# Performance work log

Measured on AMD Instinct MI355X. Metric: run time of the kernel, lower is better.

The kernel has to match this reference:

```python
import jax, jax.numpy as jnp
import numpy as np

B = 64        # number of graphs
NPG = 2048    # nodes per graph (equal-size; math identical to padded ragged original)
N = B * NPG
C = 64        # in_channels == out_channels
H = 4         # num_heads
D = 64        # out_channels per head


def setup_inputs() -> dict:
    key = jax.random.key(0)
    k1, k2, k3, k4, k5 = jax.random.split(key, 5)
    s = 1.0 / np.sqrt(C)
    return {
        "x": jax.random.normal(k1, (N, C), dtype=jnp.float32),
        "Wq_w": jax.random.uniform(k2, (H * D, C), jnp.float32, -s, s),
        "Wq_b": jax.random.uniform(k3, (H * D,), jnp.float32, -s, s),
        "Wk_w": jax.random.uniform(k4, (H * D, C), jnp.float32, -s, s),
        "Wk_b": jax.random.uniform(k5, (H * D,), jnp.float32, -s, s),
        "n_nodes": jnp.full((B,), NPG, dtype=jnp.int32),
    }


def reference(x, Wq_w, Wq_b, Wk_w, Wk_b, n_nodes):
    # Linear projections (torch Linear: x @ W^T + b), reshape to [N, H, D]
    q = (x @ Wq_w.T + Wq_b).reshape(N, H, D)
    k = (x @ Wk_w.T + Wk_b).reshape(N, H, D)
    v = jnp.broadcast_to(x[:, None, :], (N, H, C))  # value = x repeated per head

    # L2-normalize q, k along feature dim
    q = q / jnp.linalg.norm(q, axis=2, keepdims=True)
    k = k / jnp.linalg.norm(k, axis=2, keepdims=True)

    # segment views: [B, n, H, D]
    qb = q.reshape(B, NPG, H, D)
    kb = k.reshape(B, NPG, H, D)
    vb = v.reshape(B, NPG, H, C)

    # per-graph k^T v outer product: [B, H, D, C]
    kv = jnp.einsum('bnhd,bnhe->bhde', kb, vb)
    k_sum = kb.sum(axis=1)  # [B, H, D]
    v_sum = vb.sum(axis=1)  # [B, H, C]

    numerator = jnp.einsum('bnhd,bhde->bnhe', qb, kv) + v_sum[:, None]  # [B, n, H, C]
    nn = n_nodes.astype(x.dtype)
    denominator = jnp.einsum('bnhd,bhd->bnh', qb, k_sum) + nn[:, None, None]  # [B, n, H]

    out = numerator / denominator[..., None]
    return out.reshape(N, H * C)
```

## Files before the change

### kernel.cpp

```cpp
#include <hip/hip_runtime.h>

#define NPG    2048
#define XP     72
#define TP     136
#define KVTSZ  6400

typedef short bf16x8 __attribute__((ext_vector_type(8)));
typedef float f32x4  __attribute__((ext_vector_type(4)));
typedef unsigned short u16x8 __attribute__((ext_vector_type(8)));
typedef unsigned short u16x4 __attribute__((ext_vector_type(4)));

__device__ __forceinline__ unsigned short f2b(float f) {
    unsigned int u = __float_as_uint(f);
    return (unsigned short)((u + 0x7FFFu + ((u >> 16) & 1u)) >> 16);
}

extern "C" __global__ __launch_bounds__(512, 4)
void kv_kernel(const float* __restrict__ x,
               const float* __restrict__ Wk_w,
               const float* __restrict__ Wk_b,
               float* __restrict__ kvt)
{
    __shared__ __align__(16) unsigned short wlds[64 * XP];
    __shared__ __align__(16) unsigned short xlds[128 * XP];
    __shared__ __align__(16) unsigned short xt[80 * TP];
    __shared__ __align__(16) unsigned short kt[80 * TP];

    const int t  = threadIdx.x;
    const int l  = t & 63;
    const int w  = t >> 6;
    const int lr = l & 15;
    const int lg = l >> 4;
    const int g    = blockIdx.x;
    const int xcd  = g & 7;
    const int rest = g >> 3;
    const int bhi  = rest & 7;
    const int h     = (rest >> 3) & 3;
    const int chunk = rest >> 5;
    const int b     = bhi * 8 + xcd;
    const int bh    = b * 4 + h;

    for (int idx = t; idx < 64 * 64; idx += 512) {
        int r = idx >> 6, c = idx & 63;
        wlds[r * XP + c] = f2b(Wk_w[(size_t)(h * 64 + r) * 64 + c]);
    }
    float bias[4][4];
#pragma unroll
    for (int mt = 0; mt < 4; ++mt)
#pragma unroll
        for (int i = 0; i < 4; ++i) bias[mt][i] = Wk_b[h * 64 + mt * 16 + 4 * lg + i];

    for (int idx = t; idx < 16 * TP; idx += 512) {
        int rr = idx / TP;
        int cc = idx - rr * TP;
        unsigned short v = (rr == 0 && cc < 128) ? (unsigned short)0x3F80u : (unsigned short)0u;
        xt[(64 + rr) * TP + cc] = v;
        kt[(64 + rr) * TP + cc] = v;
    }

    int cts[4], dts[4];
#pragma unroll
    for (int ti = 0; ti < 3; ++ti) {
        int tau = w + 8 * ti;
        int q5  = tau / 5;
        cts[ti] = q5;
        dts[ti] = tau - 5 * q5;
    }
    cts[3] = 4; dts[3] = 4;

    f32x4 kvacc[4] = {};
    const int cpc = t & 63;
    const int n0  = (t >> 6) * 16;

    const float4* xg0 = (const float4*)(x + ((size_t)b * NPG + (size_t)chunk * 1024) * 64);

    float4 rx[4];
#pragma unroll
    for (int j = 0; j < 4; ++j) rx[j] = xg0[j * 512 + t];
#pragma unroll
    for (int j = 0; j < 4; ++j) {
        int n = j * 32 + (t >> 4), c = (t & 15) * 4;
        u16x4 pv = { f2b(rx[j].x), f2b(rx[j].y), f2b(rx[j].z), f2b(rx[j].w) };
        *(u16x4*)&xlds[n * XP + c] = pv;
    }
    __syncthreads();

    for (int tt = 0; tt < 8; ++tt) {
        {
            u16x8 w0, w1;
#pragma unroll
            for (int k2 = 0; k2 < 8; ++k2) w0[k2] = xlds[(n0 + k2) * XP + cpc];
#pragma unroll
            for (int k2 = 0; k2 < 8; ++k2) w1[k2] = xlds[(n0 + 8 + k2) * XP + cpc];
            *(u16x8*)&xt[cpc * TP + n0]     = w0;
            *(u16x8*)&xt[cpc * TP + n0 + 8] = w1;
        }

        f32x4 pacc[4] = {};
        const int ncol = w * 16 + lr;
#pragma unroll
        for (int ks = 0; ks < 2; ++ks) {
            bf16x8 xb = *(const bf16x8*)&xlds[ncol * XP + ks * 32 + lg * 8];
#pragma unroll
            for (int mt = 0; mt < 4; ++mt) {
                bf16x8 wfr = *(const bf16x8*)&wlds[(mt * 16 + lr) * XP + ks * 32 + lg * 8];
                pacc[mt] = __builtin_amdgcn_mfma_f32_16x16x32_bf16(wfr, xb, pacc[mt], 0, 0, 0);
            }
        }
        float ss = 0.f;
#pragma unroll
        for (int mt = 0; mt < 4; ++mt)
#pragma unroll
            for (int i = 0; i < 4; ++i) {
                float v = pacc[mt][i] + bias[mt][i];
                pacc[mt][i] = v;
                ss = fmaf(v, v, ss);
            }
        ss += __shfl_xor(ss, 16, 64);
        ss += __shfl_xor(ss, 32, 64);
        float sc = rsqrtf(ss);
#pragma unroll
        for (int mt = 0; mt < 4; ++mt)
#pragma unroll
            for (int i = 0; i < 4; ++i)
                kt[(mt * 16 + 4 * lg + i) * TP + ncol] = f2b(pacc[mt][i] * sc);
        __syncthreads();

        const bool more = (tt + 1) < 8;
        if (more) {
            const float4* xg = xg0 + (size_t)(tt + 1) * 128 * 16;
#pragma unroll
            for (int j = 0; j < 4; ++j) rx[j] = xg[j * 512 + t];
        }

#pragma unroll
        for (int ks = 0; ks < 4; ++ks) {
            const int ko = ks * 32 + lg * 8;
            bf16x8 a0 = *(const bf16x8*)&xt[(cts[0] * 16 + lr) * TP + ko];
            bf16x8 b0 = *(const bf16x8*)&kt[(dts[0] * 16 + lr) * TP + ko];
            kvacc[0] = __builtin_amdgcn_mfma_f32_16x16x32_bf16(a0, b0, kvacc[0], 0, 0, 0);
            bf16x8 a1 = *(const bf16x8*)&xt[(cts[1] * 16 + lr) * TP + ko];
            bf16x8 b1 = *(const bf16x8*)&kt[(dts[1] * 16 + lr) * TP + ko];
            kvacc[1] = __builtin_amdgcn_mfma_f32_16x16x32_bf16(a1, b1, kvacc[1], 0, 0, 0);
            bf16x8 a2 = *(const bf16x8*)&xt[(cts[2] * 16 + lr) * TP + ko];
            bf16x8 b2 = *(const bf16x8*)&kt[(dts[2] * 16 + lr) * TP + ko];
            kvacc[2] = __builtin_amdgcn_mfma_f32_16x16x32_bf16(a2, b2, kvacc[2], 0, 0, 0);
            if (w == 0) {
                bf16x8 a3 = *(const bf16x8*)&xt[(64 + lr) * TP + ko];
                bf16x8 b3 = *(const bf16x8*)&kt[(64 + lr) * TP + ko];
                kvacc[3] = __builtin_amdgcn_mfma_f32_16x16x32_bf16(a3, b3, kvacc[3], 0, 0, 0);
            }
        }

        if (more) {
#pragma unroll
            for (int j = 0; j < 4; ++j) {
                int n = j * 32 + (t >> 4), c = (t & 15) * 4;
                u16x4 pv = { f2b(rx[j].x), f2b(rx[j].y), f2b(rx[j].z), f2b(rx[j].w) };
                *(u16x4*)&xlds[n * XP + c] = pv;
            }
        }
        __syncthreads();
    }

    float* base = kvt + (size_t)(chunk * 256 + bh) * KVTSZ;
#pragma unroll
    for (int ti = 0; ti < 3; ++ti) {
        float* dst = base + (size_t)(cts[ti] * 16 + 4 * lg) * 80 + dts[ti] * 16 + lr;
#pragma unroll
        for (int i = 0; i < 4; ++i) dst[i * 80] = kvacc[ti][i];
    }
    if (w == 0) {
        float* dst = base + (size_t)(64 + 4 * lg) * 80 + 64 + lr;
#pragma unroll
        for (int i = 0; i < 4; ++i) dst[i * 80] = kvacc[3][i];
    }
}

extern "C" __global__ __launch_bounds__(256)
void out_kernel(const float* __restrict__ x,
                const float* __restrict__ Wq_w,
                const float* __restrict__ Wq_b,
                const int* __restrict__ n_nodes,
                const float* __restrict__ kvt,
                float* __restrict__ out)
{
    __shared__ __align__(16) unsigned short wlds[64 * XP];

    const int t  = threadIdx.x;
    const int l  = t & 63;
    const int w  = t >> 6;
    const int lr = l & 15;
    const int lg = l >> 4;
    const int g    = blockIdx.x;
    const int xcd  = g & 7;
    const int r    = g >> 3;
    const int bhi  = r & 7;
    const int hq   = r >> 3;
    const int h    = hq & 3;
    const int quarter = hq >> 2;
    const int b    = bhi * 8 + xcd;
    const int bh   = b * 4 + h;
    const int chunk = quarter * 4 + w;

    for (int idx = t; idx < 64 * 64; idx += 256) {
        int rr = idx >> 6, c = idx & 63;
        wlds[rr * XP + c] = f2b(Wq_w[(size_t)(h * 64 + rr) * 64 + c]);
    }
    float bias[4][4];
#pragma unroll
    for (int mt = 0; mt < 4; ++mt)
#pragma unroll
        for (int i = 0; i < 4; ++i) bias[mt][i] = Wq_b[h * 64 + mt * 16 + 4 * lg + i];

    const float* kp0 = kvt + (size_t)bh * KVTSZ;
    const float* kp1 = kp0 + (size_t)256 * KVTSZ;
    bf16x8 kvf[4][2];
#pragma unroll
    for (int ct = 0; ct < 4; ++ct)
#pragma unroll
        for (int ks = 0; ks < 2; ++ks) {
            const int o = (ct * 16 + lr) * 80 + ks * 32 + lg * 8;
            bf16x8 f;
#pragma unroll
            for (int j = 0; j < 8; ++j) f[j] = (short)f2b(kp0[o + j] + kp1[o + j]);
            kvf[ct][ks] = f;
        }
    float ksr[4][4];
#pragma unroll
    for (int mt = 0; mt < 4; ++mt)
#pragma unroll
        for (int i = 0; i < 4; ++i) {
            const int d = mt * 16 + 4 * lg + i;
            ksr[mt][i] = kp0[64 * 80 + d] + kp1[64 * 80 + d];
        }
    float vsr[4];
#pragma unroll
    for (int ct = 0; ct < 4; ++ct) {
        const int o = (ct * 16 + lr) * 80 + 64;
        vsr[ct] = kp0[o] + kp1[o];
    }
    const float npg = (float)n_nodes[b];

    __syncthreads();

    const float* xbase = x + ((size_t)b * NPG + (size_t)chunk * 128) * 64;
    const int src0 = lr + 16 * ((lg & 1) * 2);
    const int src1 = src0 + 16;

    for (int gg = 0; gg < 8; ++gg) {
        const float* xr = xbase + (size_t)(gg * 16 + lr) * 64;
        bf16x8 xb[2];
#pragma unroll
        for (int ks = 0; ks < 2; ++ks) {
            float4 p0 = *(const float4*)(xr + ks * 32 + lg * 8);
            float4 p1 = *(const float4*)(xr + ks * 32 + lg * 8 + 4);
            bf16x8 f;
            f[0] = (short)f2b(p0.x); f[1] = (short)f2b(p0.y);
            f[2] = (short)f2b(p0.z); f[3] = (short)f2b(p0.w);
            f[4] = (short)f2b(p1.x); f[5] = (short)f2b(p1.y);
            f[6] = (short)f2b(p1.z); f[7] = (short)f2b(p1.w);
            xb[ks] = f;
        }

        f32x4 pacc[4] = {};
#pragma unroll
        for (int ks = 0; ks < 2; ++ks)
#pragma unroll
            for (int mt = 0; mt < 4; ++mt) {
                bf16x8 wfr = *(const bf16x8*)&wlds[(mt * 16 + lr) * XP + ks * 32 + lg * 8];
                pacc[mt] = __builtin_amdgcn_mfma_f32_16x16x32_bf16(wfr, xb[ks], pacc[mt], 0, 0, 0);
            }

        float ss = 0.f, dd = 0.f;
#pragma unroll
        for (int mt = 0; mt < 4; ++mt)
#pragma unroll
            for (int i = 0; i < 4; ++i) {
                float v = pacc[mt][i] + bias[mt][i];
                pacc[mt][i] = v;
                ss = fmaf(v, v, ss);
                dd = fmaf(v, ksr[mt][i], dd);
            }
        ss += __shfl_xor(ss, 16, 64);
        ss += __shfl_xor(ss, 32, 64);
        dd += __shfl_xor(dd, 16, 64);
        dd += __shfl_xor(dd, 32, 64);
        const float sc  = rsqrtf(ss);
        const float den = fmaf(dd, sc, npg);

        unsigned pw[4][2];
#pragma unroll
        for (int mt = 0; mt < 4; ++mt) {
            pw[mt][0] = (unsigned)f2b(pacc[mt][0] * sc) | ((unsigned)f2b(pacc[mt][1] * sc) << 16);
            pw[mt][1] = (unsigned)f2b(pacc[mt][2] * sc) | ((unsigned)f2b(pacc[mt][3] * sc) << 16);
        }

        unsigned r0[4][2], r1[4][2];
#pragma unroll
        for (int mt = 0; mt < 4; ++mt)
#pragma unroll
            for (int p = 0; p < 2; ++p) {
                r0[mt][p] = __shfl(pw[mt][p], src0, 64);
                r1[mt][p] = __shfl(pw[mt][p], src1, 64);
            }
        const bool hi = (lg >> 1) & 1;
        union { unsigned u[4]; bf16x8 v; } a0, a1;
        a0.u[0] = hi ? r0[1][0] : r0[0][0];
        a0.u[1] = hi ? r0[1][1] : r0[0][1];
        a0.u[2] = hi ? r1[1][0] : r1[0][0];
        a0.u[3] = hi ? r1[1][1] : r1[0][1];
        a1.u[0] = hi ? r0[3][0] : r0[2][0];
        a1.u[1] = hi ? r0[3][1] : r0[2][1];
        a1.u[2] = hi ? r1[3][0] : r1[2][0];
        a1.u[3] = hi ? r1[3][1] : r1[2][1];

        f32x4 nacc[4] = {};
#pragma unroll
        for (int ct = 0; ct < 4; ++ct) {
            nacc[ct] = __builtin_amdgcn_mfma_f32_16x16x32_bf16(a0.v, kvf[ct][0], nacc[ct], 0, 0, 0);
            nacc[ct] = __builtin_amdgcn_mfma_f32_16x16x32_bf16(a1.v, kvf[ct][1], nacc[ct], 0, 0, 0);
        }

        float* op = out + ((size_t)b * NPG + (size_t)chunk * 128 + gg * 16) * 256 + h * 64;
#pragma unroll
        for (int i = 0; i < 4; ++i) {
            const float den_i = __shfl(den, 4 * lg + i, 64);
            const float rd = 1.0f / den_i;
#pragma unroll
            for (int ct = 0; ct < 4; ++ct)
                op[(size_t)(4 * lg + i) * 256 + ct * 16 + lr] = (nacc[ct][i] + vsr[ct]) * rd;
        }
    }
}

extern "C" void kernel_launch(void* const* d_in, const int* in_sizes, int n_in,
                              void* d_out, int out_size, void* d_ws, size_t ws_size,
                              hipStream_t stream) {
    const float* x     = (const float*)d_in[0];
    const float* Wq_w  = (const float*)d_in[1];
    const float* Wq_b  = (const float*)d_in[2];
    const float* Wk_w  = (const float*)d_in[3];
    const float* Wk_b  = (const float*)d_in[4];
    const int* n_nodes = (const int*)d_in[5];
    float* out = (float*)d_out;
    float* kvt = (float*)d_ws;

    hipLaunchKernelGGL(kv_kernel,  dim3(512),  dim3(512), 0, stream, x, Wk_w, Wk_b, kvt);
    hipLaunchKernelGGL(out_kernel, dim3(1024), dim3(256), 0, stream, x, Wq_w, Wq_b, n_nodes, kvt, out);
}
```

Before: 223.7 us.

## Compute normalized Q in the KV kernel and stream bf16 Q to output pass

Moves the Q projection and normalization into the first kernel, which already holds x tiles in LDS, and writes normalized Q as bf16 to a workspace buffer. The second kernel then only reads Q, the KV partials and the sums. Node chunks are split four ways instead of two, which doubles the first kernel's grid. k_sum and v_sum now come from separate shuffle reductions rather than padded ones-rows in the MFMA. This removes the second x read and the duplicate projection from the output kernel, but adds a 64 MB bf16 Q write and read plus more partial KV traffic.

```diff
diff --git a/kernel.cpp b/kernel.cpp
--- a/kernel.cpp
+++ b/kernel.cpp
@@ -1,9 +1,8 @@
 #include <hip/hip_runtime.h>
 
-#define NPG    2048
-#define XP     72
-#define TP     136
-#define KVTSZ  6400
+#define NPG   2048
+#define XP    72
+#define TP    136
 
 typedef short bf16x8 __attribute__((ext_vector_type(8)));
 typedef float f32x4  __attribute__((ext_vector_type(4)));
@@ -14,17 +13,26 @@
     unsigned int u = __float_as_uint(f);
     return (unsigned short)((u + 0x7FFFu + ((u >> 16) & 1u)) >> 16);
 }
+__device__ __forceinline__ float b2f(unsigned short u) {
+    return __uint_as_float((unsigned)u << 16);
+}
 
 extern "C" __global__ __launch_bounds__(512, 4)
 void kv_kernel(const float* __restrict__ x,
-               const float* __restrict__ Wk_w,
-               const float* __restrict__ Wk_b,
-               float* __restrict__ kvt)
+               const float* __restrict__ Wk_w, const float* __restrict__ Wk_b,
+               const float* __restrict__ Wq_w, const float* __restrict__ Wq_b,
+               unsigned short* __restrict__ qbuf,
+               float* __restrict__ kvp, float* __restrict__ ksump,
+               float* __restrict__ vsump)
 {
-    __shared__ __align__(16) unsigned short wlds[64 * XP];
+    __shared__ __align__(16) unsigned short wk[64 * XP];
+    __shared__ __align__(16) unsigned short wq[64 * XP];
     __shared__ __align__(16) unsigned short xlds[128 * XP];
-    __shared__ __align__(16) unsigned short xt[80 * TP];
-    __shared__ __align__(16) unsigned short kt[80 * TP];
+    __shared__ __align__(16) unsigned short xt[64 * TP];
+    __shared__ __align__(16) unsigned short kt[64 * TP];
+    __shared__ __align__(16) float blds[128];
+    __shared__ float kred[8][64];
+    __shared__ float vred[8][64];
 
     const int t  = threadIdx.x;
     const int l  = t & 63;
@@ -42,37 +50,29 @@
 
     for (int idx = t; idx < 64 * 64; idx += 512) {
         int r = idx >> 6, c = idx & 63;
-        wlds[r * XP + c] = f2b(Wk_w[(size_t)(h * 64 + r) * 64 + c]);
-    }
-    float bias[4][4];
-#pragma unroll
-    for (int mt = 0; mt < 4; ++mt)
-#pragma unroll
-        for (int i = 0; i < 4; ++i) bias[mt][i] = Wk_b[h * 64 + mt * 16 + 4 * lg + i];
-
-    for (int idx = t; idx < 16 * TP; idx += 512) {
-        int rr = idx / TP;
-        int cc = idx - rr * TP;
-        unsigned short v = (rr == 0 && cc < 128) ? (unsigned short)0x3F80u : (unsigned short)0u;
-        xt[(64 + rr) * TP + cc] = v;
-        kt[(64 + rr) * TP + cc] = v;
-    }
-
-    int cts[4], dts[4];
-#pragma unroll
-    for (int ti = 0; ti < 3; ++ti) {
-        int tau = w + 8 * ti;
-        int q5  = tau / 5;
-        cts[ti] = q5;
-        dts[ti] = tau - 5 * q5;
-    }
-    cts[3] = 4; dts[3] = 4;
-
-    f32x4 kvacc[4] = {};
+        wk[r * XP + c] = f2b(Wk_w[(size_t)(h * 64 + r) * 64 + c]);
+        wq[r * XP + c] = f2b(Wq_w[(size_t)(h * 64 + r) * 64 + c]);
+    }
+    if (t < 64) {
+        blds[t]      = Wk_b[h * 64 + t];
+        blds[64 + t] = Wq_b[h * 64 + t];
+    }
+
+    const int ct  = w >> 1;
+    const int dt0 = (w & 1) * 2;
+    const int dt1 = dt0 + 1;
+    f32x4 kvacc[2] = {};
+    float ksacc[4][4] = {};
+    float vsacc[4] = {};
+
     const int cpc = t & 63;
     const int n0  = (t >> 6) * 16;
-
-    const float4* xg0 = (const float4*)(x + ((size_t)b * NPG + (size_t)chunk * 1024) * 64);
+    const int src0 = lr + ((lg & 1) * 32);
+    const int src1 = src0 + 16;
+    const bool hi  = (lg >> 1) & 1;
+
+    const size_t node_base = (size_t)b * NPG + (size_t)chunk * 512;
+    const float4* xg0 = (const float4*)(x + node_base * 64);
 
     float4 rx[4];
 #pragma unroll
@@ -82,10 +82,12 @@
         int n = j * 32 + (t >> 4), c = (t & 15) * 4;
         u16x4 pv = { f2b(rx[j].x), f2b(rx[j].y), f2b(rx[j].z), f2b(rx[j].w) };
         *(u16x4*)&xlds[n * XP + c] = pv;
+        vsacc[0] += rx[j].x; vsacc[1] += rx[j].y;
+        vsacc[2] += rx[j].z; vsacc[3] += rx[j].w;
     }
     __syncthreads();
 
-    for (int tt = 0; tt < 8; ++tt) {
+    for (int tt = 0; tt < 4; ++tt) {
         {
             u16x8 w0, w1;
 #pragma unroll
@@ -96,37 +98,101 @@
             *(u16x8*)&xt[cpc * TP + n0 + 8] = w1;
         }
 
-        f32x4 pacc[4] = {};
         const int ncol = w * 16 + lr;
-#pragma unroll
-        for (int ks = 0; ks < 2; ++ks) {
-            bf16x8 xb = *(const bf16x8*)&xlds[ncol * XP + ks * 32 + lg * 8];
+        bf16x8 xb[2];
+#pragma unroll
+        for (int ks = 0; ks < 2; ++ks)
+            xb[ks] = *(const bf16x8*)&xlds[ncol * XP + ks * 32 + lg * 8];
+
+        {
+            f32x4 pacc[4] = {};
+#pragma unroll
+            for (int ks = 0; ks < 2; ++ks)
+#pragma unroll
+                for (int mt = 0; mt < 4; ++mt) {
+                    bf16x8 wfr = *(const bf16x8*)&wk[(mt * 16 + lr) * XP + ks * 32 + lg * 8];
+                    pacc[mt] = __builtin_amdgcn_mfma_f32_16x16x32_bf16(wfr, xb[ks], pacc[mt], 0, 0, 0);
+                }
+            float ss = 0.f;
 #pragma unroll
             for (int mt = 0; mt < 4; ++mt) {
-                bf16x8 wfr = *(const bf16x8*)&wlds[(mt * 16 + lr) * XP + ks * 32 + lg * 8];
-                pacc[mt] = __builtin_amdgcn_mfma_f32_16x16x32_bf16(wfr, xb, pacc[mt], 0, 0, 0);
-            }
-        }
-        float ss = 0.f;
-#pragma unroll
-        for (int mt = 0; mt < 4; ++mt)
-#pragma unroll
-            for (int i = 0; i < 4; ++i) {
-                float v = pacc[mt][i] + bias[mt][i];
-                pacc[mt][i] = v;
-                ss = fmaf(v, v, ss);
-            }
-        ss += __shfl_xor(ss, 16, 64);
-        ss += __shfl_xor(ss, 32, 64);
-        float sc = rsqrtf(ss);
-#pragma unroll
-        for (int mt = 0; mt < 4; ++mt)
-#pragma unroll
-            for (int i = 0; i < 4; ++i)
-                kt[(mt * 16 + 4 * lg + i) * TP + ncol] = f2b(pacc[mt][i] * sc);
+                f32x4 bk = *(const f32x4*)&blds[mt * 16 + 4 * lg];
+#pragma unroll
+                for (int i = 0; i < 4; ++i) {
+                    float v = pacc[mt][i] + bk[i];
+                    pacc[mt][i] = v;
+                    ss = fmaf(v, v, ss);
+                }
+            }
+            ss += __shfl_xor(ss, 16, 64);
+            ss += __shfl_xor(ss, 32, 64);
+            const float sc = rsqrtf(ss);
+#pragma unroll
+            for (int mt = 0; mt < 4; ++mt)
+#pragma unroll
+                for (int i = 0; i < 4; ++i) {
+                    float kn = pacc[mt][i] * sc;
+                    ksacc[mt][i] += kn;
+                    kt[(mt * 16 + 4 * lg + i) * TP + ncol] = f2b(kn);
+                }
+        }
+
+        {
+            f32x4 pacc[4] = {};
+#pragma unroll
+            for (int ks = 0; ks < 2; ++ks)
+#pragma unroll
+                for (int mt = 0; mt < 4; ++mt) {
+                    bf16x8 wfr = *(const bf16x8*)&wq[(mt * 16 + lr) * XP + ks * 32 + lg * 8];
+                    pacc[mt] = __builtin_amdgcn_mfma_f32_16x16x32_bf16(wfr, xb[ks], pacc[mt], 0, 0, 0);
+                }
+            float ss = 0.f;
+#pragma unroll
+            for (int mt = 0; mt < 4; ++mt) {
+                f32x4 bq = *(const f32x4*)&blds[64 + mt * 16 + 4 * lg];
+#pragma unroll
+                for (int i = 0; i < 4; ++i) {
+                    float v = pacc[mt][i] + bq[i];
+                    pacc[mt][i] = v;
+                    ss = fmaf(v, v, ss);
+                }
+            }
+            ss += __shfl_xor(ss, 16, 64);
+            ss += __shfl_xor(ss, 32, 64);
+            const float sc = rsqrtf(ss);
+
+            unsigned pw[4][2];
+#pragma unroll
+            for (int mt = 0; mt < 4; ++mt) {
+                pw[mt][0] = (unsigned)f2b(pacc[mt][0] * sc) | ((unsigned)f2b(pacc[mt][1] * sc) << 16);
+                pw[mt][1] = (unsigned)f2b(pacc[mt][2] * sc) | ((unsigned)f2b(pacc[mt][3] * sc) << 16);
+            }
+            unsigned r0[4][2], r1[4][2];
+#pragma unroll
+            for (int mt = 0; mt < 4; ++mt)
+#pragma unroll
+                for (int p = 0; p < 2; ++p) {
+                    r0[mt][p] = __shfl(pw[mt][p], src0, 64);
+                    r1[mt][p] = __shfl(pw[mt][p], src1, 64);
+                }
+            union { unsigned u[4]; u16x8 v; } a0, a1;
+            a0.u[0] = hi ? r0[1][0] : r0[0][0];
+            a0.u[1] = hi ? r0[1][1] : r0[0][1];
+            a0.u[2] = hi ? r1[1][0] : r1[0][0];
+            a0.u[3] = hi ? r1[1][1] : r1[0][1];
+            a1.u[0] = hi ? r0[3][0] : r0[2][0];
+            a1.u[1] = hi ? r0[3][1] : r0[2][1];
+            a1.u[2] = hi ? r1[3][0] : r1[2][0];
+            a1.u[3] = hi ? r1[3][1] : r1[2][1];
+
+            const size_t node = node_base + (size_t)tt * 128 + ncol;
+            unsigned short* qp = qbuf + node * 256 + h * 64 + lg * 8;
+            *(u16x8*)qp        = a0.v;
+            *(u16x8*)(qp + 32) = a1.v;
+        }
         __syncthreads();
 
-        const bool more = (tt + 1) < 8;
+        const bool more = (tt + 1) < 4;
         if (more) {
             const float4* xg = xg0 + (size_t)(tt + 1) * 128 * 16;
 #pragma unroll
@@ -136,20 +202,11 @@
 #pragma unroll
         for (int ks = 0; ks < 4; ++ks) {
             const int ko = ks * 32 + lg * 8;
-            bf16x8 a0 = *(const bf16x8*)&xt[(cts[0] * 16 + lr) * TP + ko];
-            bf16x8 b0 = *(const bf16x8*)&kt[(dts[0] * 16 + lr) * TP + ko];
-            kvacc[0] = __builtin_amdgcn_mfma_f32_16x16x32_bf16(a0, b0, kvacc[0], 0, 0, 0);
-            bf16x8 a1 = *(const bf16x8*)&xt[(cts[1] * 16 + lr) * TP + ko];
-            bf16x8 b1 = *(const bf16x8*)&kt[(dts[1] * 16 + lr) * TP + ko];
-            kvacc[1] = __builtin_amdgcn_mfma_f32_16x16x32_bf16(a1, b1, kvacc[1], 0, 0, 0);
-            bf16x8 a2 = *(const bf16x8*)&xt[(cts[2] * 16 + lr) * TP + ko];
-            bf16x8 b2 = *(const bf16x8*)&kt[(dts[2] * 16 + lr) * TP + ko];
-            kvacc[2] = __builtin_amdgcn_mfma_f32_16x16x32_bf16(a2, b2, kvacc[2], 0, 0, 0);
-            if (w == 0) {
-                bf16x8 a3 = *(const bf16x8*)&xt[(64 + lr) * TP + ko];
-                bf16x8 b3 = *(const bf16x8*)&kt[(64 + lr) * TP + ko];
-                kvacc[3] = __builtin_amdgcn_mfma_f32_16x16x32_bf16(a3, b3, kvacc[3], 0, 0, 0);
-            }
+            bf16x8 a  = *(const bf16x8*)&xt[(ct  * 16 + lr) * TP + ko];
+            bf16x8 b0 = *(const bf16x8*)&kt[(dt0 * 16 + lr) * TP + ko];
+            bf16x8 b1 = *(const bf16x8*)&kt[(dt1 * 16 + lr) * TP + ko];
+            kvacc[0] = __builtin_amdgcn_mfma_f32_16x16x32_bf16(a, b0, kvacc[0], 0, 0, 0);
+            kvacc[1] = __builtin_amdgcn_mfma_f32_16x16x32_bf16(a, b1, kvacc[1], 0, 0, 0);
         }
 
         if (more) {
@@ -158,35 +215,60 @@
                 int n = j * 32 + (t >> 4), c = (t & 15) * 4;
                 u16x4 pv = { f2b(rx[j].x), f2b(rx[j].y), f2b(rx[j].z), f2b(rx[j].w) };
                 *(u16x4*)&xlds[n * XP + c] = pv;
+                vsacc[0] += rx[j].x; vsacc[1] += rx[j].y;
+                vsacc[2] += rx[j].z; vsacc[3] += rx[j].w;
             }
         }
         __syncthreads();
     }
 
-    float* base = kvt + (size_t)(chunk * 256 + bh) * KVTSZ;
-#pragma unroll
-    for (int ti = 0; ti < 3; ++ti) {
-        float* dst = base + (size_t)(cts[ti] * 16 + 4 * lg) * 80 + dts[ti] * 16 + lr;
-#pragma unroll
-        for (int i = 0; i < 4; ++i) dst[i * 80] = kvacc[ti][i];
-    }
-    if (w == 0) {
-        float* dst = base + (size_t)(64 + 4 * lg) * 80 + 64 + lr;
-#pragma unroll
-        for (int i = 0; i < 4; ++i) dst[i * 80] = kvacc[3][i];
-    }
-}
-
-extern "C" __global__ __launch_bounds__(256)
-void out_kernel(const float* __restrict__ x,
-                const float* __restrict__ Wq_w,
-                const float* __restrict__ Wq_b,
+#pragma unroll
+    for (int mt = 0; mt < 4; ++mt)
+#pragma unroll
+        for (int i = 0; i < 4; ++i) {
+            float v = ksacc[mt][i];
+            v += __shfl_xor(v, 1, 64);
+            v += __shfl_xor(v, 2, 64);
+            v += __shfl_xor(v, 4, 64);
+            v += __shfl_xor(v, 8, 64);
+            if (lr == 0) kred[w][mt * 16 + 4 * lg + i] = v;
+        }
+#pragma unroll
+    for (int j = 0; j < 4; ++j) {
+        float v = vsacc[j];
+        v += __shfl_xor(v, 16, 64);
+        v += __shfl_xor(v, 32, 64);
+        if (lg == 0) vred[w][lr * 4 + j] = v;
+    }
+    __syncthreads();
+
+    float* kvbase = kvp + ((size_t)chunk * 256 + bh) * 4096;
+#pragma unroll
+    for (int i = 0; i < 4; ++i) {
+        kvbase[(size_t)(ct * 16 + 4 * lg + i) * 64 + dt0 * 16 + lr] = kvacc[0][i];
+        kvbase[(size_t)(ct * 16 + 4 * lg + i) * 64 + dt1 * 16 + lr] = kvacc[1][i];
+    }
+    if (t < 64) {
+        float s = 0.f;
+#pragma unroll
+        for (int ww = 0; ww < 8; ++ww) s += kred[ww][t];
+        ksump[((size_t)chunk * 256 + bh) * 64 + t] = s;
+        if (h == 0) {
+            float s2 = 0.f;
+#pragma unroll
+            for (int ww = 0; ww < 8; ++ww) s2 += vred[ww][t];
+            vsump[((size_t)chunk * 64 + b) * 64 + t] = s2;
+        }
+    }
+}
+
+extern "C" __global__ __launch_bounds__(256, 4)
+void out_kernel(const unsigned short* __restrict__ qbuf,
                 const int* __restrict__ n_nodes,
-                const float* __restrict__ kvt,
+                const float* __restrict__ kvp, const float* __restrict__ ksump,
+                const float* __restrict__ vsump,
                 float* __restrict__ out)
 {
-    __shared__ __align__(16) unsigned short wlds[64 * XP];
-
     const int t  = threadIdx.x;
     const int l  = t & 63;
     const int w  = t >> 6;
@@ -203,133 +285,82 @@
     const int bh   = b * 4 + h;
     const int chunk = quarter * 4 + w;
 
-    for (int idx = t; idx < 64 * 64; idx += 256) {
-        int rr = idx >> 6, c = idx & 63;
-        wlds[rr * XP + c] = f2b(Wq_w[(size_t)(h * 64 + rr) * 64 + c]);
-    }
-    float bias[4][4];
-#pragma unroll
-    for (int mt = 0; mt < 4; ++mt)
-#pragma unroll
-        for (int i = 0; i < 4; ++i) bias[mt][i] = Wq_b[h * 64 + mt * 16 + 4 * lg + i];
-
-    const float* kp0 = kvt + (size_t)bh * KVTSZ;
-    const float* kp1 = kp0 + (size_t)256 * KVTSZ;
     bf16x8 kvf[4][2];
 #pragma unroll
-    for (int ct = 0; ct < 4; ++ct)
+    for (int ctc = 0; ctc < 4; ++ctc)
 #pragma unroll
         for (int ks = 0; ks < 2; ++ks) {
-            const int o = (ct * 16 + lr) * 80 + ks * 32 + lg * 8;
+            f32x4 s0 = {}, s1 = {};
+#pragma unroll
+            for (int p = 0; p < 4; ++p) {
+                const float* kp = kvp + ((size_t)p * 256 + bh) * 4096
+                                + (size_t)(ctc * 16 + lr) * 64 + ks * 32 + lg * 8;
+                s0 += *(const f32x4*)kp;
+                s1 += *(const f32x4*)(kp + 4);
+            }
             bf16x8 f;
 #pragma unroll
-            for (int j = 0; j < 8; ++j) f[j] = (short)f2b(kp0[o + j] + kp1[o + j]);
-            kvf[ct][ks] = f;
-        }
-    float ksr[4][4];
-#pragma unroll
-    for (int mt = 0; mt < 4; ++mt)
-#pragma unroll
-        for (int i = 0; i < 4; ++i) {
-            const int d = mt * 16 + 4 * lg + i;
-            ksr[mt][i] = kp0[64 * 80 + d] + kp1[64 * 80 + d];
+            for (int j = 0; j < 4; ++j) f[j]     = (short)f2b(s0[j]);
+#pragma unroll
+            for (int j = 0; j < 4; ++j) f[4 + j] = (short)f2b(s1[j]);
+            kvf[ctc][ks] = f;
+        }
+    float ksr[16];
+#pragma unroll
+    for (int ks = 0; ks < 2; ++ks)
+#pragma unroll
+        for (int j = 0; j < 8; ++j) {
+            const int d = ks * 32 + lg * 8 + j;
+            float s = 0.f;
+#pragma unroll
+            for (int p = 0; p < 4; ++p)
+                s += ksump[((size_t)p * 256 + bh) * 64 + d];
+            ksr[ks * 8 + j] = s;
         }
     float vsr[4];
 #pragma unroll
-    for (int ct = 0; ct < 4; ++ct) {
-        const int o = (ct * 16 + lr) * 80 + 64;
-        vsr[ct] = kp0[o] + kp1[o];
+    for (int ctc = 0; ctc < 4; ++ctc) {
+        float s = 0.f;
+#pragma unroll
+        for (int p = 0; p < 4; ++p)
+            s += vsump[((size_t)p * 64 + b) * 64 + ctc * 16 + lr];
+        vsr[ctc] = s;
     }
     const float npg = (float)n_nodes[b];
 
-    __syncthreads();
-
-    const float* xbase = x + ((size_t)b * NPG + (size_t)chunk * 128) * 64;
-    const int src0 = lr + 16 * ((lg & 1) * 2);
-    const int src1 = src0 + 16;
+    const size_t node_base = (size_t)b * NPG + (size_t)chunk * 128;
 
     for (int gg = 0; gg < 8; ++gg) {
-        const float* xr = xbase + (size_t)(gg * 16 + lr) * 64;
-        bf16x8 xb[2];
-#pragma unroll
-        for (int ks = 0; ks < 2; ++ks) {
-            float4 p0 = *(const float4*)(xr + ks * 32 + lg * 8);
-            float4 p1 = *(const float4*)(xr + ks * 32 + lg * 8 + 4);
-            bf16x8 f;
-            f[0] = (short)f2b(p0.x); f[1] = (short)f2b(p0.y);
-            f[2] = (short)f2b(p0.z); f[3] = (short)f2b(p0.w);
-            f[4] = (short)f2b(p1.x); f[5] = (short)f2b(p1.y);
-            f[6] = (short)f2b(p1.z); f[7] = (short)f2b(p1.w);
-            xb[ks] = f;
-        }
-
-        f32x4 pacc[4] = {};
-#pragma unroll
-        for (int ks = 0; ks < 2; ++ks)
-#pragma unroll
-            for (int mt = 0; mt < 4; ++mt) {
-                bf16x8 wfr = *(const bf16x8*)&wlds[(mt * 16 + lr) * XP + ks * 32 + lg * 8];
-                pacc[mt] = __builtin_amdgcn_mfma_f32_16x16x32_bf16(wfr, xb[ks], pacc[mt], 0, 0, 0);
-            }
-
-        float ss = 0.f, dd = 0.f;
-#pragma unroll
-        for (int mt = 0; mt < 4; ++mt)
-#pragma unroll
-            for (int i = 0; i < 4; ++i) {
-                float v = pacc[mt][i] + bias[mt][i];
-                pacc[mt][i] = v;
-                ss = fmaf(v, v, ss);
-                dd = fmaf(v, ksr[mt][i], dd);
-            }
-        ss += __shfl_xor(ss, 16, 64);
-        ss += __shfl_xor(ss, 32, 64);
-        dd += __shfl_xor(dd, 16, 64);
-        dd += __shfl_xor(dd, 32, 64);
-        const float sc  = rsqrtf(ss);
-        const float den = fmaf(dd, sc, npg);
-
-        unsigned pw[4][2];
-#pragma unroll
-        for (int mt = 0; mt < 4; ++mt) {
-            pw[mt][0] = (unsigned)f2b(pacc[mt][0] * sc) | ((unsigned)f2b(pacc[mt][1] * sc) << 16);
-            pw[mt][1] = (unsigned)f2b(pacc[mt][2] * sc) | ((unsigned)f2b(pacc[mt][3] * sc) << 16);
-        }
-
-        unsigned r0[4][2], r1[4][2];
-#pragma unroll
-        for (int mt = 0; mt < 4; ++mt)
-#pragma unroll
-            for (int p = 0; p < 2; ++p) {
-                r0[mt][p] = __shfl(pw[mt][p], src0, 64);
-                r1[mt][p] = __shfl(pw[mt][p], src1, 64);
-            }
-        const bool hi = (lg >> 1) & 1;
-        union { unsigned u[4]; bf16x8 v; } a0, a1;
-        a0.u[0] = hi ? r0[1][0] : r0[0][0];
-        a0.u[1] = hi ? r0[1][1] : r0[0][1];
-        a0.u[2] = hi ? r1[1][0] : r1[0][0];
-        a0.u[3] = hi ? r1[1][1] : r1[0][1];
-        a1.u[0] = hi ? r0[3][0] : r0[2][0];
-        a1.u[1] = hi ? r0[3][1] : r0[2][1];
-        a1.u[2] = hi ? r1[3][0] : r1[2][0];
-        a1.u[3] = hi ? r1[3][1] : r1[2][1];
+        const size_t node = node_base + gg * 16 + lr;
+        const unsigned short* qp = qbuf + node * 256 + h * 64 + lg * 8;
+        bf16x8 qa0 = *(const bf16x8*)qp;
+        bf16x8 qa1 = *(const bf16x8*)(qp + 32);
+
+        float den = 0.f;
+#pragma unroll
+        for (int j = 0; j < 8; ++j) {
+            den = fmaf(b2f((unsigned short)qa0[j]), ksr[j],     den);
+            den = fmaf(b2f((unsigned short)qa1[j]), ksr[8 + j], den);
+        }
+        den += __shfl_xor(den, 16, 64);
+        den += __shfl_xor(den, 32, 64);
+        den += npg;
 
         f32x4 nacc[4] = {};
 #pragma unroll
-        for (int ct = 0; ct < 4; ++ct) {
-            nacc[ct] = __builtin_amdgcn_mfma_f32_16x16x32_bf16(a0.v, kvf[ct][0], nacc[ct], 0, 0, 0);
-            nacc[ct] = __builtin_amdgcn_mfma_f32_16x16x32_bf16(a1.v, kvf[ct][1], nacc[ct], 0, 0, 0);
-        }
-
-        float* op = out + ((size_t)b * NPG + (size_t)chunk * 128 + gg * 16) * 256 + h * 64;
+        for (int ctc = 0; ctc < 4; ++ctc) {
+            nacc[ctc] = __builtin_amdgcn_mfma_f32_16x16x32_bf16(qa0, kvf[ctc][0], nacc[ctc], 0, 0, 0);
+            nacc[ctc] = __builtin_amdgcn_mfma_f32_16x16x32_bf16(qa1, kvf[ctc][1], nacc[ctc], 0, 0, 0);
+        }
+
+        float* op = out + (node_base + gg * 16) * 256 + h * 64;
 #pragma unroll
         for (int i = 0; i < 4; ++i) {
             const float den_i = __shfl(den, 4 * lg + i, 64);
             const float rd = 1.0f / den_i;
 #pragma unroll
-            for (int ct = 0; ct < 4; ++ct)
-                op[(size_t)(4 * lg + i) * 256 + ct * 16 + lr] = (nacc[ct][i] + vsr[ct]) * rd;
+            for (int ctc = 0; ctc < 4; ++ctc)
+                op[(size_t)(4 * lg + i) * 256 + ctc * 16 + lr] = (nacc[ctc][i] + vsr[ctc]) * rd;
         }
     }
 }
@@ -344,8 +375,14 @@
     const float* Wk_b  = (const float*)d_in[4];
     const int* n_nodes = (const int*)d_in[5];
     float* out = (float*)d_out;
-    float* kvt = (float*)d_ws;
-
-    hipLaunchKernelGGL(kv_kernel,  dim3(512),  dim3(512), 0, stream, x, Wk_w, Wk_b, kvt);
-    hipLaunchKernelGGL(out_kernel, dim3(1024), dim3(256), 0, stream, x, Wq_w, Wq_b, n_nodes, kvt, out);
-}
+
+    unsigned short* qbuf = (unsigned short*)d_ws;
+    float* kvp  = (float*)((char*)d_ws + (size_t)67108864);
+    float* ksum = kvp + (size_t)4 * 256 * 4096;
+    float* vsum = ksum + (size_t)4 * 256 * 64;
+
+    hipLaunchKernelGGL(kv_kernel, dim3(1024), dim3(512), 0, stream,
+                       x, Wk_w, Wk_b, Wq_w, Wq_b, qbuf, kvp, ksum, vsum);
+    hipLaunchKernelGGL(out_kernel, dim3(1024), dim3(256), 0, stream,
+                       qbuf, n_nodes, kvp, ksum, vsum, out);
+}
```

Measured after the change: 264.5 us. +18.2%, slower.
